# Kernel tuning notes

Hardware: AMD Instinct MI355X
Metric: run time of the kernel (lower is better)

Reference implementation:

```python
import jax, jax.numpy as jnp
import numpy as np

N_NODES = 50000
N_EDGES = 800000
D_FEAT = 64
H = 128


def scatter_mean(x, idx, num_segments):
    # mean of x rows per segment; empty segments -> 0 (matches torch_scatter scatter_mean)
    s = jax.ops.segment_sum(x, idx, num_segments=num_segments)
    c = jax.ops.segment_sum(jnp.ones((x.shape[0],), dtype=x.dtype), idx, num_segments=num_segments)
    return s / jnp.maximum(c, 1.0)[:, None]


def setup_inputs() -> dict:
    key = jax.random.key(0)
    ks = jax.random.split(key, 6)
    edge_attr = jax.random.normal(ks[0], (N_EDGES, D_FEAT), dtype=jnp.float32)
    edge_index = jax.random.randint(ks[1], (2, N_EDGES), 0, N_NODES, dtype=jnp.int64 if jax.config.jax_enable_x64 else jnp.int32)
    # ensure max index == N_NODES - 1 so num_nodes inference matches
    edge_index = edge_index.at[0, 0].set(N_NODES - 1)
    sc = 0.05
    W0 = jax.random.normal(ks[2], (D_FEAT + D_FEAT, H), dtype=jnp.float32) * sc
    b0 = jnp.zeros((H,), dtype=jnp.float32)
    W1 = jax.random.normal(ks[3], (H + D_FEAT, H), dtype=jnp.float32) * sc
    b1 = jnp.zeros((H,), dtype=jnp.float32)
    Wf = jax.random.normal(ks[4], (2 * H, 1), dtype=jnp.float32) * sc
    bf = jnp.zeros((1,), dtype=jnp.float32)
    return {"edge_attr": edge_attr, "edge_index": edge_index,
            "W0": W0, "b0": b0, "W1": W1, "b1": b1, "Wf": Wf, "bf": bf}


def reference(edge_attr, edge_index, W0, b0, W1, b1, Wf, bf):
    src = edge_index[0]
    dst = edge_index[1]
    # initial node features: mean of incoming edge_attr over edge_index[1]
    node_attr = scatter_mean(edge_attr, dst, N_NODES)            # [N, D_FEAT]
    # layer 0: aggregate over edge_index[0], concat, linear, sigmoid
    agg = scatter_mean(edge_attr, src, N_NODES)                  # [N, D_FEAT]
    node_attr = jax.nn.sigmoid(jnp.concatenate([node_attr, agg], axis=1) @ W0 + b0)  # [N, H]
    # layer 1
    agg = scatter_mean(edge_attr, src, N_NODES)                  # [N, D_FEAT]
    node_attr = jax.nn.sigmoid(jnp.concatenate([node_attr, agg], axis=1) @ W1 + b1)  # [N, H]
    # final edge classifier: gather endpoints, concat, linear
    edge_embs = jnp.concatenate([node_attr[src], node_attr[dst]], axis=1)  # [E, 2H]
    embeddings = jax.lax.stop_gradient(edge_embs)
    logits = (edge_embs @ Wf + bf).reshape(-1)                   # [E]
    return logits, embeddings
```

## Files before the change

### kernel.cpp

```cpp
#include <hip/hip_runtime.h>
#include <hip/hip_bf16.h>

#define N_NODES 50000
#define N_EDGES 800000
#define D_FEAT 64
#define H 128
#define CAP 96

typedef float f32x4 __attribute__((ext_vector_type(4)));

__global__ void k_fill(const int* __restrict__ ei,
                       int* __restrict__ cnt_dst, int* __restrict__ cnt_src,
                       int* __restrict__ bkt_dst, int* __restrict__ bkt_src) {
    int t = blockIdx.x * blockDim.x + threadIdx.x;
    if (t >= N_EDGES / 4) return;
    int4 s = ((const int4*)ei)[t];
    int4 d = ((const int4*)(ei + N_EDGES))[t];
    int e = 4 * t;
    int p;
    p = atomicAdd(&cnt_src[s.x], 1); if (p < CAP) bkt_src[(size_t)s.x * CAP + p] = e;
    p = atomicAdd(&cnt_src[s.y], 1); if (p < CAP) bkt_src[(size_t)s.y * CAP + p] = e + 1;
    p = atomicAdd(&cnt_src[s.z], 1); if (p < CAP) bkt_src[(size_t)s.z * CAP + p] = e + 2;
    p = atomicAdd(&cnt_src[s.w], 1); if (p < CAP) bkt_src[(size_t)s.w * CAP + p] = e + 3;
    p = atomicAdd(&cnt_dst[d.x], 1); if (p < CAP) bkt_dst[(size_t)d.x * CAP + p] = e;
    p = atomicAdd(&cnt_dst[d.y], 1); if (p < CAP) bkt_dst[(size_t)d.y * CAP + p] = e + 1;
    p = atomicAdd(&cnt_dst[d.z], 1); if (p < CAP) bkt_dst[(size_t)d.z * CAP + p] = e + 2;
    p = atomicAdd(&cnt_dst[d.w], 1); if (p < CAP) bkt_dst[(size_t)d.w * CAP + p] = e + 3;
}

__global__ __launch_bounds__(128) void k_node(const float* __restrict__ ea,
        const int* __restrict__ cnt_dst, const int* __restrict__ bkt_dst,
        const int* __restrict__ cnt_src, const int* __restrict__ bkt_src,
        const float* __restrict__ W0, const float* __restrict__ b0,
        const float* __restrict__ W1, const float* __restrict__ b1,
        float* __restrict__ h1) {
    __shared__ float x0[16][128];
    __shared__ float x1[16][192];
    int t = threadIdx.x;
    int n0 = blockIdx.x * 16;
    {
        int unit = t >> 2;
        int l = t & 3;
        int nn = unit >> 1;
        int dir = unit & 1;
        int n = n0 + nn;
        const int* cnt = dir ? cnt_src : cnt_dst;
        const int* bkt = dir ? bkt_src : bkt_dst;
        int c = cnt[n];
        size_t b = (size_t)n * CAP;
        f32x4 a0 = {0.f,0.f,0.f,0.f}, a1 = {0.f,0.f,0.f,0.f};
        f32x4 a2 = {0.f,0.f,0.f,0.f}, a3 = {0.f,0.f,0.f,0.f};
        int i = 0;
        for (; i + 2 <= c; i += 2) {
            int e0 = bkt[b + i];
            int e1 = bkt[b + i + 1];
            const float* r0 = ea + (size_t)e0 * D_FEAT;
            const float* r1 = ea + (size_t)e1 * D_FEAT;
            f32x4 u0 = *(const f32x4*)(r0 + 4 * l);
            f32x4 u1 = *(const f32x4*)(r0 + 4 * l + 16);
            f32x4 u2 = *(const f32x4*)(r0 + 4 * l + 32);
            f32x4 u3 = *(const f32x4*)(r0 + 4 * l + 48);
            f32x4 w0 = *(const f32x4*)(r1 + 4 * l);
            f32x4 w1 = *(const f32x4*)(r1 + 4 * l + 16);
            f32x4 w2 = *(const f32x4*)(r1 + 4 * l + 32);
            f32x4 w3 = *(const f32x4*)(r1 + 4 * l + 48);
            a0 += u0; a1 += u1; a2 += u2; a3 += u3;
            a0 += w0; a1 += w1; a2 += w2; a3 += w3;
        }
        if (i < c) {
            int e0 = bkt[b + i];
            const float* r0 = ea + (size_t)e0 * D_FEAT;
            a0 += *(const f32x4*)(r0 + 4 * l);
            a1 += *(const f32x4*)(r0 + 4 * l + 16);
            a2 += *(const f32x4*)(r0 + 4 * l + 32);
            a3 += *(const f32x4*)(r0 + 4 * l + 48);
        }
        float dinv = 1.0f / fmaxf((float)c, 1.0f);
        a0 *= dinv; a1 *= dinv; a2 *= dinv; a3 *= dinv;
        float* xr = &x0[nn][dir * 64 + 4 * l];
        *(f32x4*)(xr)      = a0;
        *(f32x4*)(xr + 16) = a1;
        *(f32x4*)(xr + 32) = a2;
        *(f32x4*)(xr + 48) = a3;
        if (dir) {
            float* yr = &x1[nn][128 + 4 * l];
            *(f32x4*)(yr)      = a0;
            *(f32x4*)(yr + 16) = a1;
            *(f32x4*)(yr + 32) = a2;
            *(f32x4*)(yr + 48) = a3;
        }
    }
    __syncthreads();
    {
        float acc[16];
        float bias = b0[t];
        #pragma unroll
        for (int n = 0; n < 16; n++) acc[n] = bias;
        for (int k = 0; k < 128; k += 4) {
            float w0 = W0[(k + 0) * 128 + t];
            float w1 = W0[(k + 1) * 128 + t];
            float w2 = W0[(k + 2) * 128 + t];
            float w3 = W0[(k + 3) * 128 + t];
            #pragma unroll
            for (int n = 0; n < 16; n++) {
                f32x4 xv = *(const f32x4*)&x0[n][k];
                acc[n] = fmaf(xv.x, w0, acc[n]);
                acc[n] = fmaf(xv.y, w1, acc[n]);
                acc[n] = fmaf(xv.z, w2, acc[n]);
                acc[n] = fmaf(xv.w, w3, acc[n]);
            }
        }
        #pragma unroll
        for (int n = 0; n < 16; n++) x1[n][t] = 1.0f / (1.0f + __expf(-acc[n]));
    }
    __syncthreads();
    {
        float acc[16];
        float bias = b1[t];
        #pragma unroll
        for (int n = 0; n < 16; n++) acc[n] = bias;
        for (int k = 0; k < 192; k += 4) {
            float w0 = W1[(k + 0) * 128 + t];
            float w1 = W1[(k + 1) * 128 + t];
            float w2 = W1[(k + 2) * 128 + t];
            float w3 = W1[(k + 3) * 128 + t];
            #pragma unroll
            for (int n = 0; n < 16; n++) {
                f32x4 xv = *(const f32x4*)&x1[n][k];
                acc[n] = fmaf(xv.x, w0, acc[n]);
                acc[n] = fmaf(xv.y, w1, acc[n]);
                acc[n] = fmaf(xv.z, w2, acc[n]);
                acc[n] = fmaf(xv.w, w3, acc[n]);
            }
        }
        #pragma unroll
        for (int n = 0; n < 16; n++)
            h1[(size_t)(n0 + n) * 128 + t] = 1.0f / (1.0f + __expf(-acc[n]));
    }
}

__global__ void k_emb(const float* __restrict__ h1,
                      const int* __restrict__ cnt_src, const int* __restrict__ bkt_src,
                      const int* __restrict__ cnt_dst, const int* __restrict__ bkt_dst,
                      const float* __restrict__ Wf,
                      float* __restrict__ emb, float* __restrict__ ps, float* __restrict__ pd) {
    int gid = blockIdx.x * blockDim.x + threadIdx.x;
    int wid = gid >> 6;
    int lane = gid & 63;
    if (wid >= 2 * N_NODES) return;
    int n, half;
    const int* cnt;
    const int* bkt;
    float* pout;
    if (wid < N_NODES) { n = wid;           half = 0; cnt = cnt_src; bkt = bkt_src; pout = ps; }
    else               { n = wid - N_NODES; half = 1; cnt = cnt_dst; bkt = bkt_dst; pout = pd; }
    int q = lane & 31;
    f32x4 v = *(const f32x4*)(h1 + (size_t)n * 128 + q * 4);
    {
        f32x4 w = *(const f32x4*)(Wf + half * 128 + q * 4);
        float p = v.x * w.x + v.y * w.y + v.z * w.z + v.w * w.w;
        p += __shfl_xor(p, 1, 64);
        p += __shfl_xor(p, 2, 64);
        p += __shfl_xor(p, 4, 64);
        p += __shfl_xor(p, 8, 64);
        p += __shfl_xor(p, 16, 64);
        if (lane == 0) pout[n] = p;
    }
    int c = cnt[n];
    size_t base = (size_t)n * CAP;
    int sub = lane >> 5;
    size_t boff = (size_t)half * 128 + q * 4;
    int i = sub;
    for (; i + 2 < c; i += 4) {
        int ea = bkt[base + i];
        int eb = bkt[base + i + 2];
        __builtin_nontemporal_store(v, (f32x4*)(emb + (size_t)ea * 256 + boff));
        __builtin_nontemporal_store(v, (f32x4*)(emb + (size_t)eb * 256 + boff));
    }
    for (; i < c; i += 2) {
        int ea = bkt[base + i];
        __builtin_nontemporal_store(v, (f32x4*)(emb + (size_t)ea * 256 + boff));
    }
}

__global__ void k_logits(const int* __restrict__ ei, const float* __restrict__ ps,
                         const float* __restrict__ pd, const float* __restrict__ bfp,
                         float* __restrict__ logits) {
    int e = blockIdx.x * blockDim.x + threadIdx.x;
    if (e >= N_EDGES) return;
    float r = ps[ei[e]] + pd[ei[N_EDGES + e]] + bfp[0];
    __builtin_nontemporal_store(r, &logits[e]);
}

extern "C" void kernel_launch(void* const* d_in, const int* in_sizes, int n_in,
                              void* d_out, int out_size, void* d_ws, size_t ws_size,
                              hipStream_t stream) {
    const float* edge_attr  = (const float*)d_in[0];
    const int*   edge_index = (const int*)d_in[1];
    const float* W0  = (const float*)d_in[2];
    const float* b0  = (const float*)d_in[3];
    const float* W1  = (const float*)d_in[4];
    const float* b1  = (const float*)d_in[5];
    const float* Wf  = (const float*)d_in[6];
    const float* bfp = (const float*)d_in[7];

    float* out = (float*)d_out;
    float* logits = out;
    float* emb    = out + N_EDGES;

    float* ws = (float*)d_ws;
    float* h1      = ws;
    float* ps      = ws + 6400000;
    float* pd      = ps + 50000;
    int*   cnt_dst = (int*)(pd + 50000);
    int*   cnt_src = cnt_dst + 50000;
    int*   bkt_dst = cnt_src + 50000;
    int*   bkt_src = bkt_dst + (size_t)N_NODES * CAP;

    hipMemsetAsync(cnt_dst, 0, 2 * N_NODES * sizeof(int), stream);

    {
        int grid = (N_EDGES / 4 + 255) / 256;
        k_fill<<<grid, 256, 0, stream>>>(edge_index, cnt_dst, cnt_src, bkt_dst, bkt_src);
    }
    {
        k_node<<<3125, 128, 0, stream>>>(edge_attr, cnt_dst, bkt_dst, cnt_src, bkt_src,
                                         W0, b0, W1, b1, h1);
    }
    {
        long long total = (long long)2 * N_NODES * 64;
        int grid = (int)((total + 255) / 256);
        k_emb<<<grid, 256, 0, stream>>>(h1, cnt_src, bkt_src, cnt_dst, bkt_dst,
                                        Wf, emb, ps, pd);
    }
    {
        k_logits<<<3125, 256, 0, stream>>>(edge_index, ps, pd, bfp, logits);
    }
}
```

Before: 442.5 us.

## Fuse embedding scatter and logit projections into node MLP kernel

Drops the separate k_emb kernel and the h1 workspace round trip. The node kernel now keeps the final hidden activations in registers, computes the per-node Wf projections with wave shuffles, stages each node's edge lists in shared memory, and scatters 4-byte per-thread embedding stores directly. Bucket counts are clamped to CAP. The scatter stores are now scalar rather than 16-byte vectors, and the larger per-block tail work may lower occupancy or imbalance load.

```diff
diff --git a/kernel.cpp b/kernel.cpp
--- a/kernel.cpp
+++ b/kernel.cpp
@@ -33,11 +33,15 @@
         const int* __restrict__ cnt_src, const int* __restrict__ bkt_src,
         const float* __restrict__ W0, const float* __restrict__ b0,
         const float* __restrict__ W1, const float* __restrict__ b1,
-        float* __restrict__ h1) {
+        const float* __restrict__ Wf,
+        float* __restrict__ emb, float* __restrict__ ps, float* __restrict__ pd) {
     __shared__ float x0[16][128];
     __shared__ float x1[16][192];
+    __shared__ float red[16][2][2];
+    __shared__ int ccnt[32];
     int t = threadIdx.x;
     int n0 = blockIdx.x * 16;
+
     {
         int unit = t >> 2;
         int l = t & 3;
@@ -47,11 +51,12 @@
         const int* cnt = dir ? cnt_src : cnt_dst;
         const int* bkt = dir ? bkt_src : bkt_dst;
         int c = cnt[n];
+        int cc = c < CAP ? c : CAP;
         size_t b = (size_t)n * CAP;
         f32x4 a0 = {0.f,0.f,0.f,0.f}, a1 = {0.f,0.f,0.f,0.f};
         f32x4 a2 = {0.f,0.f,0.f,0.f}, a3 = {0.f,0.f,0.f,0.f};
         int i = 0;
-        for (; i + 2 <= c; i += 2) {
+        for (; i + 2 <= cc; i += 2) {
             int e0 = bkt[b + i];
             int e1 = bkt[b + i + 1];
             const float* r0 = ea + (size_t)e0 * D_FEAT;
@@ -67,7 +72,7 @@
             a0 += u0; a1 += u1; a2 += u2; a3 += u3;
             a0 += w0; a1 += w1; a2 += w2; a3 += w3;
         }
-        if (i < c) {
+        if (i < cc) {
             int e0 = bkt[b + i];
             const float* r0 = ea + (size_t)e0 * D_FEAT;
             a0 += *(const f32x4*)(r0 + 4 * l);
@@ -89,6 +94,7 @@
             *(f32x4*)(yr + 32) = a2;
             *(f32x4*)(yr + 48) = a3;
         }
+        if (l == 0) ccnt[unit] = cc;
     }
     __syncthreads();
     {
@@ -114,6 +120,7 @@
         for (int n = 0; n < 16; n++) x1[n][t] = 1.0f / (1.0f + __expf(-acc[n]));
     }
     __syncthreads();
+    float hv[16];
     {
         float acc[16];
         float bias = b1[t];
@@ -134,52 +141,57 @@
             }
         }
         #pragma unroll
-        for (int n = 0; n < 16; n++)
-            h1[(size_t)(n0 + n) * 128 + t] = 1.0f / (1.0f + __expf(-acc[n]));
-    }
-}
-
-__global__ void k_emb(const float* __restrict__ h1,
-                      const int* __restrict__ cnt_src, const int* __restrict__ bkt_src,
-                      const int* __restrict__ cnt_dst, const int* __restrict__ bkt_dst,
-                      const float* __restrict__ Wf,
-                      float* __restrict__ emb, float* __restrict__ ps, float* __restrict__ pd) {
-    int gid = blockIdx.x * blockDim.x + threadIdx.x;
-    int wid = gid >> 6;
-    int lane = gid & 63;
-    if (wid >= 2 * N_NODES) return;
-    int n, half;
-    const int* cnt;
-    const int* bkt;
-    float* pout;
-    if (wid < N_NODES) { n = wid;           half = 0; cnt = cnt_src; bkt = bkt_src; pout = ps; }
-    else               { n = wid - N_NODES; half = 1; cnt = cnt_dst; bkt = bkt_dst; pout = pd; }
-    int q = lane & 31;
-    f32x4 v = *(const f32x4*)(h1 + (size_t)n * 128 + q * 4);
-    {
-        f32x4 w = *(const f32x4*)(Wf + half * 128 + q * 4);
-        float p = v.x * w.x + v.y * w.y + v.z * w.z + v.w * w.w;
-        p += __shfl_xor(p, 1, 64);
-        p += __shfl_xor(p, 2, 64);
-        p += __shfl_xor(p, 4, 64);
-        p += __shfl_xor(p, 8, 64);
-        p += __shfl_xor(p, 16, 64);
-        if (lane == 0) pout[n] = p;
-    }
-    int c = cnt[n];
-    size_t base = (size_t)n * CAP;
-    int sub = lane >> 5;
-    size_t boff = (size_t)half * 128 + q * 4;
-    int i = sub;
-    for (; i + 2 < c; i += 4) {
-        int ea = bkt[base + i];
-        int eb = bkt[base + i + 2];
-        __builtin_nontemporal_store(v, (f32x4*)(emb + (size_t)ea * 256 + boff));
-        __builtin_nontemporal_store(v, (f32x4*)(emb + (size_t)eb * 256 + boff));
-    }
-    for (; i < c; i += 2) {
-        int ea = bkt[base + i];
-        __builtin_nontemporal_store(v, (f32x4*)(emb + (size_t)ea * 256 + boff));
+        for (int n = 0; n < 16; n++) hv[n] = 1.0f / (1.0f + __expf(-acc[n]));
+    }
+    {
+        float wlo = Wf[t];
+        float whi = Wf[128 + t];
+        int wv = t >> 6, ln = t & 63;
+        #pragma unroll
+        for (int n = 0; n < 16; n++) {
+            float a = hv[n] * wlo;
+            float b = hv[n] * whi;
+            #pragma unroll
+            for (int off = 32; off > 0; off >>= 1) {
+                a += __shfl_xor(a, off, 64);
+                b += __shfl_xor(b, off, 64);
+            }
+            if (ln == 0) { red[n][0][wv] = a; red[n][1][wv] = b; }
+        }
+    }
+    __syncthreads();
+    if (t < 32) {
+        int n = t >> 1, half = t & 1;
+        float v = red[n][half][0] + red[n][half][1];
+        if (half == 0) ps[n0 + n] = v; else pd[n0 + n] = v;
+    }
+    int* elist = (int*)&x1[0][0];
+    {
+        int L = t >> 2, j0 = t & 3;
+        int nn = L >> 1, dir = L & 1;
+        int n = n0 + nn;
+        const int* bkt = dir ? bkt_src : bkt_dst;
+        int c = ccnt[L];
+        for (int i = j0; i < c; i += 4)
+            elist[L * CAP + i] = bkt[(size_t)n * CAP + i];
+    }
+    __syncthreads();
+    #pragma unroll
+    for (int L = 0; L < 32; L++) {
+        int nn = L >> 1;
+        int half = 1 - (L & 1);
+        float v = hv[nn];
+        int c = ccnt[L];
+        const int* el = elist + L * CAP;
+        size_t boff = (size_t)half * 128 + t;
+        int i = 0;
+        for (; i + 1 < c; i += 2) {
+            int e0 = el[i], e1 = el[i + 1];
+            __builtin_nontemporal_store(v, emb + (size_t)e0 * 256 + boff);
+            __builtin_nontemporal_store(v, emb + (size_t)e1 * 256 + boff);
+        }
+        if (i < c)
+            __builtin_nontemporal_store(v, emb + (size_t)el[i] * 256 + boff);
     }
 }
 
@@ -209,8 +221,7 @@
     float* emb    = out + N_EDGES;
 
     float* ws = (float*)d_ws;
-    float* h1      = ws;
-    float* ps      = ws + 6400000;
+    float* ps      = ws;
     float* pd      = ps + 50000;
     int*   cnt_dst = (int*)(pd + 50000);
     int*   cnt_src = cnt_dst + 50000;
@@ -225,13 +236,7 @@
     }
     {
         k_node<<<3125, 128, 0, stream>>>(edge_attr, cnt_dst, bkt_dst, cnt_src, bkt_src,
-                                         W0, b0, W1, b1, h1);
-    }
-    {
-        long long total = (long long)2 * N_NODES * 64;
-        int grid = (int)((total + 255) / 256);
-        k_emb<<<grid, 256, 0, stream>>>(h1, cnt_src, bkt_src, cnt_dst, bkt_dst,
-                                        Wf, emb, ps, pd);
+                                         W0, b0, W1, b1, Wf, emb, ps, pd);
     }
     {
         k_logits<<<3125, 256, 0, stream>>>(edge_index, ps, pd, bfp, logits);
```

After: 427.6 us. 1.03x faster.
